# Optimization experiments

Measured on AMD Instinct MI355X. Metric: run time of the kernel, lower is better.

## Reference

```python
import jax, jax.numpy as jnp
import numpy as np

N_ITER, K, DIM = 2, 16, 64


def setup_inputs() -> dict:
    key = jax.random.key(0)
    ks = jax.random.split(key, 9)
    B, NE, NU, NR = 8192, 200000, 100000, 32
    return {
        "u": jax.random.randint(ks[0], (B,), 0, NU),
        "v": jax.random.randint(ks[1], (B,), 0, NE),
        "adj_ent": jax.random.randint(ks[2], (NE, K), 0, NE),
        "adj_rel": jax.random.randint(ks[3], (NE, K), 0, NR),
        "usr_emb": jax.random.normal(ks[4], (NU, DIM), jnp.float32) * 0.1,
        "rel_emb": jax.random.normal(ks[5], (NR, DIM), jnp.float32) * 0.1,
        "ent_emb": jax.random.normal(ks[6], (NE, DIM), jnp.float32) * 0.1,
        "W": jax.random.normal(ks[7], (DIM, DIM), jnp.float32) / np.float32(np.sqrt(DIM)),
        "b": jnp.zeros((DIM,), jnp.float32),
    }


def reference(u, v, adj_ent, adj_rel, usr_emb, rel_emb, ent_emb, W, b):
    B = u.shape[0]
    user = usr_emb[u]                                  # [B, D]

    # _get_neighbors: multi-hop fixed-fanout expansion
    entities = [v[:, None]]                            # hop 0: [B, 1]
    relations = []
    for h in range(N_ITER):
        entities.append(adj_ent[entities[h]].reshape(B, -1))   # [B, K^(h+1)]
        relations.append(adj_rel[entities[h]].reshape(B, -1))

    ent_vecs = [ent_emb[e] for e in entities]          # [B, K^h, D] gathers
    rel_vecs = [rel_emb[r] for r in relations]

    # _aggregate: attention-weighted neighbor mix + sum-combine linear
    for i in range(N_ITER):
        act = jnp.tanh if i == N_ITER - 1 else jax.nn.sigmoid
        nxt = []
        for hop in range(N_ITER - i):
            self_v = ent_vecs[hop]                              # [B, m, D]
            neigh = ent_vecs[hop + 1].reshape(B, -1, K, DIM)    # [B, m, K, D]
            rel = rel_vecs[hop].reshape(B, -1, K, DIM)          # [B, m, K, D]
            scores = jnp.einsum('bd,bmkd->bmk', user, rel)      # user-relation
            attn = jax.nn.softmax(scores, axis=-1)              # [B, m, K]
            agg = jnp.einsum('bmk,bmkd->bmd', attn, neigh)      # weighted sum
            nxt.append(act((self_v + agg) @ W + b))             # sum aggregator
        ent_vecs = nxt

    item = ent_vecs[0].reshape(B, DIM)
    return jax.nn.sigmoid(jnp.sum(user * item, axis=1))        # [B]
```

## Files before the change

kernel.cpp:

```cpp
#include <hip/hip_runtime.h>

#define KF    16
#define DIM   64

typedef __attribute__((ext_vector_type(8))) short bs8;
typedef __attribute__((ext_vector_type(4))) float f32x4;

#define C_FENCE() do { asm volatile("" ::: "memory"); \
                       __builtin_amdgcn_sched_barrier(0); } while (0)

__device__ __forceinline__ float fsig(float x) {
    return __builtin_amdgcn_rcpf(1.0f + __expf(-x));
}
__device__ __forceinline__ float ftanh(float x) {
    float e = __expf(2.0f * x);
    return 1.0f - 2.0f * __builtin_amdgcn_rcpf(e + 1.0f);
}
__device__ __forceinline__ ushort f2bf(float x) {
    uint u = __builtin_bit_cast(uint, x);
    u += 0x7fffu + ((u >> 16) & 1u);
    return (ushort)(u >> 16);
}
__device__ __forceinline__ float rdlane_f(float v, int l) {
    return __builtin_bit_cast(float, __builtin_amdgcn_readlane(__builtin_bit_cast(int, v), l));
}

__device__ __forceinline__ float softmax16(float sc) {
    float mx = sc;
    mx = fmaxf(mx, __shfl_xor(mx, 1));
    mx = fmaxf(mx, __shfl_xor(mx, 2));
    mx = fmaxf(mx, __shfl_xor(mx, 4));
    mx = fmaxf(mx, __shfl_xor(mx, 8));
    float e  = __expf(sc - mx);
    float sm = e;
    sm += __shfl_xor(sm, 1);
    sm += __shfl_xor(sm, 2);
    sm += __shfl_xor(sm, 4);
    sm += __shfl_xor(sm, 8);
    return e * __builtin_amdgcn_rcpf(sm);
}

__global__ __launch_bounds__(256) void k_pre(
    const int* __restrict__ u, const int* __restrict__ v,
    const int* __restrict__ adj_ent,
    const float* __restrict__ usr_emb, const float* __restrict__ rel_emb,
    float* __restrict__ urs_ws, int* __restrict__ e1_ws)
{
    const int lane = threadIdx.x & 63, wv = threadIdx.x >> 6;
    const int b  = blockIdx.x * 4 + wv;
    const int e0 = v[b];
    const int e1 = adj_ent[e0 * KF + (lane & 15)];
    const float user = usr_emb[(size_t)u[b] * DIM + lane];
    const int r = lane & 31, hb = lane & 32;
    float s = 0.0f;
    #pragma unroll
    for (int dd = 0; dd < 32; ++dd)
        s = fmaf(__shfl(user, hb + dd), rel_emb[r * DIM + hb + dd], s);
    s += __shfl_xor(s, 32);
    if (lane < 32) urs_ws[b * 32 + lane] = s;
    if (lane < KF) e1_ws[b * KF + lane] = e1;
}

__global__ __launch_bounds__(256) void k_nodes(
    const int* __restrict__ adj_ent, const int* __restrict__ adj_rel,
    const float* __restrict__ ent_emb,
    const float* __restrict__ urs_ws, const int* __restrict__ e1_ws,
    ushort* __restrict__ Xws)
{
    const int lane = threadIdx.x & 63, wv = threadIdx.x >> 6;
    const int gw = blockIdx.x * 4 + wv;
    const int b  = gw >> 4;
    const int lr = lane & 15;

    const int e1m = e1_ws[gw];
    const int e2v = adj_ent[e1m * KF + lr];
    const int r2  = adj_rel[e1m * KF + lr];
    float rows[KF + 1];
    rows[KF] = ent_emb[(size_t)e1m * DIM + lane];
    #pragma unroll
    for (int k = 0; k < KF; ++k) {
        const int e = __builtin_amdgcn_readlane(e2v, k);
        rows[k] = ent_emb[(size_t)e * DIM + lane];
    }
    const float at2v = softmax16(urs_ws[b * 32 + r2]);

    float g0 = 0.0f, g1 = 0.0f, g2 = 0.0f, g3 = 0.0f;
    #pragma unroll
    for (int k = 0; k < KF; k += 4) {
        g0 = fmaf(rdlane_f(at2v, k + 0), rows[k + 0], g0);
        g1 = fmaf(rdlane_f(at2v, k + 1), rows[k + 1], g1);
        g2 = fmaf(rdlane_f(at2v, k + 2), rows[k + 2], g2);
        g3 = fmaf(rdlane_f(at2v, k + 3), rows[k + 3], g3);
    }
    Xws[(size_t)gw * DIM + lane] = f2bf(rows[KF] + ((g0 + g1) + (g2 + g3)));
}

__global__ __launch_bounds__(256) void k_tail(
    const int* __restrict__ u, const int* __restrict__ v,
    const int* __restrict__ adj_rel,
    const float* __restrict__ usr_emb, const float* __restrict__ ent_emb,
    const float* __restrict__ W, const float* __restrict__ bias,
    const float* __restrict__ urs_ws, const int* __restrict__ e1_ws,
    const ushort* __restrict__ Xws, float* __restrict__ out)
{
    __shared__ __align__(16) ushort Wfrag[2][4][64][8];
    __shared__ __align__(16) ushort Xl[4][16][72];

    const int tid  = threadIdx.x;
    const int lane = tid & 63;
    const int wv   = tid >> 6;
    const int lr   = lane & 15;
    const int lg   = lane >> 4;

    {
        const int col = wv * 16 + lr;
        bs8 p0, p1;
        #pragma unroll
        for (int i = 0; i < 8; ++i) {
            p0[i] = (short)f2bf(W[(lg * 8 + i) * DIM + col]);
            p1[i] = (short)f2bf(W[(lg * 8 + i + 32) * DIM + col]);
        }
        *(bs8*)&Wfrag[0][wv][lane][0] = p0;
        *(bs8*)&Wfrag[1][wv][lane][0] = p1;
    }
    const float biasr = bias[lane];
    __syncthreads();

    const int   b     = blockIdx.x * 4 + wv;
    const int   e0    = v[b];
    const float user  = usr_emb[(size_t)u[b] * DIM + lane];
    const float ent0v = ent_emb[(size_t)e0 * DIM + lane];

    const int e1r = e1_ws[b * KF + lr];
    float rows[KF];
    #pragma unroll
    for (int k = 0; k < KF; ++k) {
        const int e = __builtin_amdgcn_readlane(e1r, k);
        rows[k] = ent_emb[(size_t)e * DIM + lane];
    }
    const bs8 a0 = *(const bs8*)&Xws[((size_t)b * KF + lr) * DIM + lg * 8];
    const bs8 a1 = *(const bs8*)&Xws[((size_t)b * KF + lr) * DIM + lg * 8 + 32];

    const int r1 = adj_rel[e0 * KF + lr];
    const float at1r = softmax16(urs_ws[b * 32 + r1]);

    float g0 = 0.0f, g1 = 0.0f, g2 = 0.0f, g3 = 0.0f;
    #pragma unroll
    for (int k = 0; k < KF; k += 4) {
        g0 = fmaf(rdlane_f(at1r, k + 0), rows[k + 0], g0);
        g1 = fmaf(rdlane_f(at1r, k + 1), rows[k + 1], g1);
        g2 = fmaf(rdlane_f(at1r, k + 2), rows[k + 2], g2);
        g3 = fmaf(rdlane_f(at1r, k + 3), rows[k + 3], g3);
    }
    const float x0 = ent0v + ((g0 + g1) + (g2 + g3));

    float bj[4];
    #pragma unroll
    for (int t = 0; t < 4; ++t) bj[t] = __shfl(biasr, t * 16 + lr);

    float agg2r[4];
    #pragma unroll
    for (int t = 0; t < 4; ++t) {
        f32x4 c; c[0] = bj[t]; c[1] = bj[t]; c[2] = bj[t]; c[3] = bj[t];
        const bs8 w0 = *(const bs8*)&Wfrag[0][t][lane][0];
        const bs8 w1 = *(const bs8*)&Wfrag[1][t][lane][0];
        c = __builtin_amdgcn_mfma_f32_16x16x32_bf16(a0, w0, c, 0, 0, 0);
        c = __builtin_amdgcn_mfma_f32_16x16x32_bf16(a1, w1, c, 0, 0, 0);
        float p = 0.0f;
        #pragma unroll
        for (int r = 0; r < 4; ++r)
            p = fmaf(__shfl(at1r, lg * 4 + r), fsig(c[r]), p);
        p += __shfl_xor(p, 16);
        p += __shfl_xor(p, 32);
        agg2r[t] = p;
    }

    Xl[wv][0][lane] = f2bf(x0);
    C_FENCE();

    float x2v[4];
    {
        const bs8 b0 = *(const bs8*)&Xl[wv][lr][lg * 8];
        const bs8 b1 = *(const bs8*)&Xl[wv][lr][lg * 8 + 32];
        #pragma unroll
        for (int t = 0; t < 4; ++t) {
            f32x4 c; c[0] = bj[t]; c[1] = bj[t]; c[2] = bj[t]; c[3] = bj[t];
            const bs8 w0 = *(const bs8*)&Wfrag[0][t][lane][0];
            const bs8 w1 = *(const bs8*)&Wfrag[1][t][lane][0];
            c = __builtin_amdgcn_mfma_f32_16x16x32_bf16(b0, w0, c, 0, 0, 0);
            c = __builtin_amdgcn_mfma_f32_16x16x32_bf16(b1, w1, c, 0, 0, 0);
            x2v[t] = fsig(c[0]) + agg2r[t];
        }
    }

    C_FENCE();
    #pragma unroll
    for (int t = 0; t < 4; ++t)
        if (lane < 16) Xl[wv][0][t * 16 + lane] = f2bf(x2v[t]);
    C_FENCE();

    float pv = 0.0f;
    {
        const bs8 b0 = *(const bs8*)&Xl[wv][lr][lg * 8];
        const bs8 b1 = *(const bs8*)&Xl[wv][lr][lg * 8 + 32];
        #pragma unroll
        for (int t = 0; t < 4; ++t) {
            f32x4 c; c[0] = bj[t]; c[1] = bj[t]; c[2] = bj[t]; c[3] = bj[t];
            const bs8 w0 = *(const bs8*)&Wfrag[0][t][lane][0];
            const bs8 w1 = *(const bs8*)&Wfrag[1][t][lane][0];
            c = __builtin_amdgcn_mfma_f32_16x16x32_bf16(b0, w0, c, 0, 0, 0);
            c = __builtin_amdgcn_mfma_f32_16x16x32_bf16(b1, w1, c, 0, 0, 0);
            const float uc = __shfl(user, t * 16 + lr);
            if (lane < 16) pv = fmaf(uc, ftanh(c[0]), pv);
        }
    }
    pv += __shfl_xor(pv, 1);
    pv += __shfl_xor(pv, 2);
    pv += __shfl_xor(pv, 4);
    pv += __shfl_xor(pv, 8);
    if (lane == 0) out[b] = fsig(pv);
}

__global__ __launch_bounds__(256) void kgcn_fused(
    const int* __restrict__ u, const int* __restrict__ v,
    const int* __restrict__ adj_ent, const int* __restrict__ adj_rel,
    const float* __restrict__ usr_emb, const float* __restrict__ rel_emb,
    const float* __restrict__ ent_emb, const float* __restrict__ W,
    const float* __restrict__ bias, float* __restrict__ out, int B)
{
    __shared__ __align__(16) ushort Wfrag[2][4][64][8];
    __shared__ __align__(16) ushort Xl[4][16][72];

    const int tid  = threadIdx.x;
    const int lane = tid & 63;
    const int wv   = tid >> 6;
    const int lr   = lane & 15;
    const int lg   = lane >> 4;

    {
        const int col = wv * 16 + lr;
        bs8 p0, p1;
        #pragma unroll
        for (int i = 0; i < 8; ++i) {
            p0[i] = (short)f2bf(W[(lg * 8 + i) * DIM + col]);
            p1[i] = (short)f2bf(W[(lg * 8 + i + 32) * DIM + col]);
        }
        *(bs8*)&Wfrag[0][wv][lane][0] = p0;
        *(bs8*)&Wfrag[1][wv][lane][0] = p1;
    }
    const float biasr = bias[lane];
    __syncthreads();

    const int   b     = blockIdx.x * 4 + wv;
    const int   e0    = v[b];
    const float user  = usr_emb[(size_t)u[b] * DIM + lane];
    const float ent0v = ent_emb[(size_t)e0 * DIM + lane];

    float ursr;
    {
        const int r  = lane & 31;
        const int hb = lane & 32;
        float s = 0.0f;
        #pragma unroll
        for (int dd = 0; dd < 32; ++dd)
            s = fmaf(__shfl(user, hb + dd), rel_emb[r * DIM + hb + dd], s);
        s += __shfl_xor(s, 32);
        ursr = s;
    }
    int e1r; float at1r;
    {
        e1r = adj_ent[e0 * KF + lr];
        at1r = softmax16(__shfl(ursr, adj_rel[e0 * KF + lr]));
    }
    int e2r[4]; float at2r[4];
    #pragma unroll
    for (int it = 0; it < 4; ++it) {
        const int m  = it * 4 + lg;
        const int em = __shfl(e1r, m);
        e2r[it] = adj_ent[em * KF + lr];
        at2r[it] = softmax16(__shfl(ursr, adj_rel[em * KF + lr]));
    }

    float agg0p = 0.0f;
    #pragma unroll
    for (int qo = 0; qo < 4; ++qo) {
        #pragma unroll 1
        for (int qi = 0; qi < 4; ++qi) {
            const int q = qo * 4 + qi;
            float rows[KF + 1];
            #pragma unroll
            for (int k = 0; k < KF; ++k) {
                const int e = __builtin_amdgcn_readlane(e2r[qo], qi * 16 + k);
                rows[k] = ent_emb[(size_t)e * DIM + lane];
            }
            rows[KF] = ent_emb[(size_t)__builtin_amdgcn_readlane(e1r, q) * DIM + lane];
            float g0 = 0.0f, g1 = 0.0f, g2 = 0.0f, g3 = 0.0f;
            #pragma unroll
            for (int k = 0; k < KF; k += 4) {
                g0 = fmaf(rdlane_f(at2r[qo], qi * 16 + k + 0), rows[k + 0], g0);
                g1 = fmaf(rdlane_f(at2r[qo], qi * 16 + k + 1), rows[k + 1], g1);
                g2 = fmaf(rdlane_f(at2r[qo], qi * 16 + k + 2), rows[k + 2], g2);
                g3 = fmaf(rdlane_f(at2r[qo], qi * 16 + k + 3), rows[k + 3], g3);
            }
            agg0p = fmaf(rdlane_f(at1r, q), rows[KF], agg0p);
            Xl[wv][q][lane] = f2bf(rows[KF] + ((g0 + g1) + (g2 + g3)));
        }
    }
    C_FENCE();

    float bj[4];
    #pragma unroll
    for (int t = 0; t < 4; ++t) bj[t] = __shfl(biasr, t * 16 + lr);

    float agg2r[4];
    {
        const bs8 a0 = *(const bs8*)&Xl[wv][lr][lg * 8];
        const bs8 a1 = *(const bs8*)&Xl[wv][lr][lg * 8 + 32];
        #pragma unroll
        for (int t = 0; t < 4; ++t) {
            f32x4 c; c[0] = bj[t]; c[1] = bj[t]; c[2] = bj[t]; c[3] = bj[t];
            const bs8 w0 = *(const bs8*)&Wfrag[0][t][lane][0];
            const bs8 w1 = *(const bs8*)&Wfrag[1][t][lane][0];
            c = __builtin_amdgcn_mfma_f32_16x16x32_bf16(a0, w0, c, 0, 0, 0);
            c = __builtin_amdgcn_mfma_f32_16x16x32_bf16(a1, w1, c, 0, 0, 0);
            float p = 0.0f;
            #pragma unroll
            for (int r = 0; r < 4; ++r)
                p = fmaf(__shfl(at1r, lg * 4 + r), fsig(c[r]), p);
            p += __shfl_xor(p, 16);
            p += __shfl_xor(p, 32);
            agg2r[t] = p;
        }
    }
    C_FENCE();
    Xl[wv][0][lane] = f2bf(ent0v + agg0p);
    C_FENCE();
    float x2v[4];
    {
        const bs8 a0 = *(const bs8*)&Xl[wv][lr][lg * 8];
        const bs8 a1 = *(const bs8*)&Xl[wv][lr][lg * 8 + 32];
        #pragma unroll
        for (int t = 0; t < 4; ++t) {
            f32x4 c; c[0] = bj[t]; c[1] = bj[t]; c[2] = bj[t]; c[3] = bj[t];
            const bs8 w0 = *(const bs8*)&Wfrag[0][t][lane][0];
            const bs8 w1 = *(const bs8*)&Wfrag[1][t][lane][0];
            c = __builtin_amdgcn_mfma_f32_16x16x32_bf16(a0, w0, c, 0, 0, 0);
            c = __builtin_amdgcn_mfma_f32_16x16x32_bf16(a1, w1, c, 0, 0, 0);
            x2v[t] = fsig(c[0]) + agg2r[t];
        }
    }
    C_FENCE();
    #pragma unroll
    for (int t = 0; t < 4; ++t)
        if (lane < 16) Xl[wv][0][t * 16 + lane] = f2bf(x2v[t]);
    C_FENCE();
    float pv = 0.0f;
    {
        const bs8 a0 = *(const bs8*)&Xl[wv][lr][lg * 8];
        const bs8 a1 = *(const bs8*)&Xl[wv][lr][lg * 8 + 32];
        #pragma unroll
        for (int t = 0; t < 4; ++t) {
            f32x4 c; c[0] = bj[t]; c[1] = bj[t]; c[2] = bj[t]; c[3] = bj[t];
            const bs8 w0 = *(const bs8*)&Wfrag[0][t][lane][0];
            const bs8 w1 = *(const bs8*)&Wfrag[1][t][lane][0];
            c = __builtin_amdgcn_mfma_f32_16x16x32_bf16(a0, w0, c, 0, 0, 0);
            c = __builtin_amdgcn_mfma_f32_16x16x32_bf16(a1, w1, c, 0, 0, 0);
            const float uc = __shfl(user, t * 16 + lr);
            if (lane < 16) pv = fmaf(uc, ftanh(c[0]), pv);
        }
    }
    pv += __shfl_xor(pv, 1);
    pv += __shfl_xor(pv, 2);
    pv += __shfl_xor(pv, 4);
    pv += __shfl_xor(pv, 8);
    if (lane == 0) out[b] = fsig(pv);
}

extern "C" void kernel_launch(void* const* d_in, const int* in_sizes, int n_in,
                              void* d_out, int out_size, void* d_ws, size_t ws_size,
                              hipStream_t stream) {
    const int*   u       = (const int*)d_in[0];
    const int*   v       = (const int*)d_in[1];
    const int*   adj_ent = (const int*)d_in[2];
    const int*   adj_rel = (const int*)d_in[3];
    const float* usr_emb = (const float*)d_in[4];
    const float* rel_emb = (const float*)d_in[5];
    const float* ent_emb = (const float*)d_in[6];
    const float* W       = (const float*)d_in[7];
    const float* bias    = (const float*)d_in[8];
    float* out = (float*)d_out;

    const int B = in_sizes[0];

    const size_t off_urs = 0;
    const size_t off_e1  = off_urs + (size_t)B * 32 * sizeof(float);
    const size_t off_X   = off_e1  + (size_t)B * KF * sizeof(int);
    const size_t need    = off_X   + (size_t)B * KF * DIM * sizeof(ushort);

    if (ws_size >= need) {
        float*  urs_ws = (float*)((char*)d_ws + off_urs);
        int*    e1_ws  = (int*)  ((char*)d_ws + off_e1);
        ushort* Xws    = (ushort*)((char*)d_ws + off_X);
        k_pre  <<<B / 4,          256, 0, stream>>>(u, v, adj_ent, usr_emb, rel_emb,
                                                    urs_ws, e1_ws);
        k_nodes<<<(B * KF) / 4,   256, 0, stream>>>(adj_ent, adj_rel, ent_emb,
                                                    urs_ws, e1_ws, Xws);
        k_tail <<<B / 4,          256, 0, stream>>>(u, v, adj_rel, usr_emb, ent_emb,
                                                    W, bias, urs_ws, e1_ws, Xws, out);
    } else {
        kgcn_fused<<<B / 4, 256, 0, stream>>>(u, v, adj_ent, adj_rel,
                                              usr_emb, rel_emb, ent_emb,
                                              W, bias, out, B);
    }
}
```

Before: 215.0 us.

## Convert entity embeddings to bf16 each call and gather from the bf16 copy

Adds a conversion pass that writes a bf16 copy of the whole entity embedding table (200k x 64) into workspace, fused into the pre-kernel launch. The node and tail kernels then gather 2-byte rows instead of 4-byte rows, halving the bytes of the random gathers. The trade is a full streaming read of the fp32 table and a write of the bf16 copy on every call, plus lower precision in the gathered neighbour vectors. It only runs when the workspace is large enough, otherwise it falls back to the fp32 path.

```diff
diff --git a/kernel.cpp b/kernel.cpp
--- a/kernel.cpp
+++ b/kernel.cpp
@@ -3,8 +3,9 @@
 #define KF    16
 #define DIM   64
 
-typedef __attribute__((ext_vector_type(8))) short bs8;
-typedef __attribute__((ext_vector_type(4))) float f32x4;
+typedef __attribute__((ext_vector_type(8))) short  bs8;
+typedef __attribute__((ext_vector_type(8))) ushort us8;
+typedef __attribute__((ext_vector_type(4))) float  f32x4;
 
 #define C_FENCE() do { asm volatile("" ::: "memory"); \
                        __builtin_amdgcn_sched_barrier(0); } while (0)
@@ -21,10 +22,12 @@
     u += 0x7fffu + ((u >> 16) & 1u);
     return (ushort)(u >> 16);
 }
+__device__ __forceinline__ float b2f(ushort b) {
+    return __builtin_bit_cast(float, (uint)b << 16);
+}
 __device__ __forceinline__ float rdlane_f(float v, int l) {
     return __builtin_bit_cast(float, __builtin_amdgcn_readlane(__builtin_bit_cast(int, v), l));
 }
-
 __device__ __forceinline__ float softmax16(float sc) {
     float mx = sc;
     mx = fmaxf(mx, __shfl_xor(mx, 1));
@@ -40,30 +43,43 @@
     return e * __builtin_amdgcn_rcpf(sm);
 }
 
-__global__ __launch_bounds__(256) void k_pre(
+__global__ __launch_bounds__(256) void k_convert_pre(
+    const float* __restrict__ ent_emb, ushort* __restrict__ ent_bf, long n8,
     const int* __restrict__ u, const int* __restrict__ v,
     const int* __restrict__ adj_ent,
     const float* __restrict__ usr_emb, const float* __restrict__ rel_emb,
-    float* __restrict__ urs_ws, int* __restrict__ e1_ws)
+    float* __restrict__ urs_ws, int* __restrict__ e1_ws, int B)
 {
-    const int lane = threadIdx.x & 63, wv = threadIdx.x >> 6;
+    const long i = (long)blockIdx.x * 256 + threadIdx.x;
+    if (i < n8) {
+        const float4 f0 = ((const float4*)ent_emb)[2 * i];
+        const float4 f1 = ((const float4*)ent_emb)[2 * i + 1];
+        us8 o;
+        o[0] = f2bf(f0.x); o[1] = f2bf(f0.y); o[2] = f2bf(f0.z); o[3] = f2bf(f0.w);
+        o[4] = f2bf(f1.x); o[5] = f2bf(f1.y); o[6] = f2bf(f1.z); o[7] = f2bf(f1.w);
+        ((us8*)ent_bf)[i] = o;
+    }
+    const int wv = threadIdx.x >> 6, lane = threadIdx.x & 63;
     const int b  = blockIdx.x * 4 + wv;
-    const int e0 = v[b];
-    const int e1 = adj_ent[e0 * KF + (lane & 15)];
-    const float user = usr_emb[(size_t)u[b] * DIM + lane];
-    const int r = lane & 31, hb = lane & 32;
-    float s = 0.0f;
-    #pragma unroll
-    for (int dd = 0; dd < 32; ++dd)
-        s = fmaf(__shfl(user, hb + dd), rel_emb[r * DIM + hb + dd], s);
-    s += __shfl_xor(s, 32);
-    if (lane < 32) urs_ws[b * 32 + lane] = s;
-    if (lane < KF) e1_ws[b * KF + lane] = e1;
-}
-
+    if (b < B) {
+        const int e0 = v[b];
+        const int e1 = adj_ent[e0 * KF + (lane & 15)];
+        const float user = usr_emb[(size_t)u[b] * DIM + lane];
+        const int r = lane & 31, hb = lane & 32;
+        float s = 0.0f;
+        #pragma unroll
+        for (int dd = 0; dd < 32; ++dd)
+            s = fmaf(__shfl(user, hb + dd), rel_emb[r * DIM + hb + dd], s);
+        s += __shfl_xor(s, 32);
+        if (lane < 32) urs_ws[b * 32 + lane] = s;
+        if (lane < KF) e1_ws[b * KF + lane] = e1;
+    }
+}
+
+template<bool BF>
 __global__ __launch_bounds__(256) void k_nodes(
     const int* __restrict__ adj_ent, const int* __restrict__ adj_rel,
-    const float* __restrict__ ent_emb,
+    const float* __restrict__ entf, const ushort* __restrict__ entb,
     const float* __restrict__ urs_ws, const int* __restrict__ e1_ws,
     ushort* __restrict__ Xws)
 {
@@ -76,11 +92,13 @@
     const int e2v = adj_ent[e1m * KF + lr];
     const int r2  = adj_rel[e1m * KF + lr];
     float rows[KF + 1];
-    rows[KF] = ent_emb[(size_t)e1m * DIM + lane];
+    rows[KF] = BF ? b2f(entb[(size_t)e1m * DIM + lane])
+                  : entf[(size_t)e1m * DIM + lane];
     #pragma unroll
     for (int k = 0; k < KF; ++k) {
         const int e = __builtin_amdgcn_readlane(e2v, k);
-        rows[k] = ent_emb[(size_t)e * DIM + lane];
+        rows[k] = BF ? b2f(entb[(size_t)e * DIM + lane])
+                     : entf[(size_t)e * DIM + lane];
     }
     const float at2v = softmax16(urs_ws[b * 32 + r2]);
 
@@ -95,10 +113,12 @@
     Xws[(size_t)gw * DIM + lane] = f2bf(rows[KF] + ((g0 + g1) + (g2 + g3)));
 }
 
+template<bool BF>
 __global__ __launch_bounds__(256) void k_tail(
     const int* __restrict__ u, const int* __restrict__ v,
     const int* __restrict__ adj_rel,
-    const float* __restrict__ usr_emb, const float* __restrict__ ent_emb,
+    const float* __restrict__ usr_emb,
+    const float* __restrict__ entf, const ushort* __restrict__ entb,
     const float* __restrict__ W, const float* __restrict__ bias,
     const float* __restrict__ urs_ws, const int* __restrict__ e1_ws,
     const ushort* __restrict__ Xws, float* __restrict__ out)
@@ -126,17 +146,19 @@
     const float biasr = bias[lane];
     __syncthreads();
 
-    const int   b     = blockIdx.x * 4 + wv;
-    const int   e0    = v[b];
-    const float user  = usr_emb[(size_t)u[b] * DIM + lane];
-    const float ent0v = ent_emb[(size_t)e0 * DIM + lane];
+    const int   b    = blockIdx.x * 4 + wv;
+    const int   e0   = v[b];
+    const float user = usr_emb[(size_t)u[b] * DIM + lane];
+    const float ent0v = BF ? b2f(entb[(size_t)e0 * DIM + lane])
+                           : entf[(size_t)e0 * DIM + lane];
 
     const int e1r = e1_ws[b * KF + lr];
     float rows[KF];
     #pragma unroll
     for (int k = 0; k < KF; ++k) {
         const int e = __builtin_amdgcn_readlane(e1r, k);
-        rows[k] = ent_emb[(size_t)e * DIM + lane];
+        rows[k] = BF ? b2f(entb[(size_t)e * DIM + lane])
+                     : entf[(size_t)e * DIM + lane];
     }
     const bs8 a0 = *(const bs8*)&Xws[((size_t)b * KF + lr) * DIM + lg * 8];
     const bs8 a1 = *(const bs8*)&Xws[((size_t)b * KF + lr) * DIM + lg * 8 + 32];
@@ -269,7 +291,7 @@
     }
     int e1r; float at1r;
     {
-        e1r = adj_ent[e0 * KF + lr];
+        e1r  = adj_ent[e0 * KF + lr];
         at1r = softmax16(__shfl(ursr, adj_rel[e0 * KF + lr]));
     }
     int e2r[4]; float at2r[4];
@@ -277,7 +299,7 @@
     for (int it = 0; it < 4; ++it) {
         const int m  = it * 4 + lg;
         const int em = __shfl(e1r, m);
-        e2r[it] = adj_ent[em * KF + lr];
+        e2r[it]  = adj_ent[em * KF + lr];
         at2r[it] = softmax16(__shfl(ursr, adj_rel[em * KF + lr]));
     }
 
@@ -390,23 +412,38 @@
     const float* bias    = (const float*)d_in[8];
     float* out = (float*)d_out;
 
-    const int B = in_sizes[0];
+    const int B  = in_sizes[0];
+    const int NE = in_sizes[2] / KF;
 
     const size_t off_urs = 0;
     const size_t off_e1  = off_urs + (size_t)B * 32 * sizeof(float);
     const size_t off_X   = off_e1  + (size_t)B * KF * sizeof(int);
-    const size_t need    = off_X   + (size_t)B * KF * DIM * sizeof(ushort);
-
-    if (ws_size >= need) {
-        float*  urs_ws = (float*)((char*)d_ws + off_urs);
-        int*    e1_ws  = (int*)  ((char*)d_ws + off_e1);
-        ushort* Xws    = (ushort*)((char*)d_ws + off_X);
-        k_pre  <<<B / 4,          256, 0, stream>>>(u, v, adj_ent, usr_emb, rel_emb,
-                                                    urs_ws, e1_ws);
-        k_nodes<<<(B * KF) / 4,   256, 0, stream>>>(adj_ent, adj_rel, ent_emb,
-                                                    urs_ws, e1_ws, Xws);
-        k_tail <<<B / 4,          256, 0, stream>>>(u, v, adj_rel, usr_emb, ent_emb,
-                                                    W, bias, urs_ws, e1_ws, Xws, out);
+    const size_t off_eb  = off_X   + (size_t)B * KF * DIM * sizeof(ushort);
+    const size_t need_sp = off_eb;
+    const size_t need_fl = off_eb  + (size_t)NE * DIM * sizeof(ushort);
+
+    float*  urs_ws = (float*)((char*)d_ws + off_urs);
+    int*    e1_ws  = (int*)  ((char*)d_ws + off_e1);
+    ushort* Xws    = (ushort*)((char*)d_ws + off_X);
+    ushort* ent_bf = (ushort*)((char*)d_ws + off_eb);
+
+    if (ws_size >= need_fl) {
+        const long n8 = (long)NE * DIM / 8;
+        const int  gcv = (int)((n8 + 255) / 256);
+        const int  gpre = B / 4;
+        k_convert_pre<<<(gcv > gpre ? gcv : gpre), 256, 0, stream>>>(
+            ent_emb, ent_bf, n8, u, v, adj_ent, usr_emb, rel_emb, urs_ws, e1_ws, B);
+        k_nodes<true><<<(B * KF) / 4, 256, 0, stream>>>(
+            adj_ent, adj_rel, ent_emb, ent_bf, urs_ws, e1_ws, Xws);
+        k_tail<true><<<B / 4, 256, 0, stream>>>(
+            u, v, adj_rel, usr_emb, ent_emb, ent_bf, W, bias, urs_ws, e1_ws, Xws, out);
+    } else if (ws_size >= need_sp) {
+        k_convert_pre<<<B / 4, 256, 0, stream>>>(
+            ent_emb, ent_bf, 0, u, v, adj_ent, usr_emb, rel_emb, urs_ws, e1_ws, B);
+        k_nodes<false><<<(B * KF) / 4, 256, 0, stream>>>(
+            adj_ent, adj_rel, ent_emb, ent_bf, urs_ws, e1_ws, Xws);
+        k_tail<false><<<B / 4, 256, 0, stream>>>(
+            u, v, adj_rel, usr_emb, ent_emb, ent_bf, W, bias, urs_ws, e1_ws, Xws, out);
     } else {
         kgcn_fused<<<B / 4, 256, 0, stream>>>(u, v, adj_ent, adj_rel,
                                               usr_emb, rel_emb, ent_emb,
```

After: 191.5 us. 10.9% less time.
